# Kernel tuning notes

Hardware: AMD Instinct MI355X
Metric: run time of the kernel (lower is better)

## Reference

```python
import jax, jax.numpy as jnp
import numpy as np

SR = 48000.0
STAB_EPS = 1e-3
BS = 32
N_FRAMES = 128
N_SAMPLES = 65536


def setup_inputs() -> dict:
    key = jax.random.key(0)
    ks = jax.random.split(key, 8)
    f0_hz = jax.random.uniform(ks[0], (BS,), minval=50.0, maxval=500.0)
    note_on_duration = jax.random.uniform(ks[1], (BS,), minval=0.3, maxval=1.0)
    phase = jax.random.uniform(ks[2], (BS,), minval=-np.pi, maxval=np.pi)
    logits = jax.random.normal(ks[3], (BS, N_FRAMES, 5))
    osc_shape = jax.random.uniform(ks[4], (BS,))
    osc_gain = jax.random.uniform(ks[5], (BS,), minval=0.5, maxval=1.0)
    dist_gain = jax.random.uniform(ks[6], (BS,), minval=1.0, maxval=4.0)
    learned_alpha = jax.random.uniform(ks[7], (BS,), minval=0.5, maxval=3.0)
    return dict(f0_hz=f0_hz, note_on_duration=note_on_duration, phase=phase,
                logits=logits, osc_shape=osc_shape, osc_gain=osc_gain,
                dist_gain=dist_gain, learned_alpha=learned_alpha,
                n_samples=N_SAMPLES)


def lin_interp_dim1(x, n_out):
    """Linear interpolation along dim 1 with align_corners=True. x: (bs, n_in, c)."""
    n_in = x.shape[1]
    pos = jnp.linspace(0.0, n_in - 1.0, n_out)
    i0 = jnp.floor(pos).astype(jnp.int32)
    i1 = jnp.minimum(i0 + 1, n_in - 1)
    frac = (pos - i0.astype(x.dtype))[None, :, None]
    return x[:, i0] * (1.0 - frac) + x[:, i1] * frac


def square_saw_vco(f0_hz, osc_shape, n_samples, phase):
    """torchsynth-style square/saw morph oscillator. f0_hz, osc_shape, phase: (bs,)."""
    f0 = f0_hz[:, None]                                   # (bs, 1)
    inc = jnp.broadcast_to(f0 / SR, (f0.shape[0], n_samples))
    arg = 2.0 * jnp.pi * jnp.cumsum(inc, axis=1) + phase[:, None]
    partials = 12000.0 / (f0 * jnp.log10(f0))
    square = jnp.tanh(jnp.pi * partials * jnp.sin(arg) / 2.0)
    s = osc_shape[:, None]
    return (1.0 - s / 2.0) * square * (1.0 + s * jnp.cos(arg / 2.0))


def exp_decay_env(alpha, note_on_duration, n_samples):
    t = jnp.arange(n_samples, dtype=jnp.float32) / SR     # (n,)
    ramp = jnp.clip(1.0 - t[None, :] / note_on_duration[:, None], STAB_EPS, 1.0)
    env = ramp ** alpha[:, None]
    return jnp.where(t[None, :] <= note_on_duration[:, None], env, 0.0)


def logits_to_a_coeff_triangle(a_logits):
    """Map 2 logits to a stable biquad denominator (a1, a2) inside the stability triangle."""
    stab = 1.0 - STAB_EPS
    a1 = 2.0 * jnp.tanh(a_logits[..., 0]) * stab
    a1_abs = jnp.abs(a1)
    a2 = ((2.0 - a1_abs) * jnp.tanh(a_logits[..., 1]) * stab + a1_abs) / 2.0
    return jnp.stack([a1, a2], axis=-1)


def sample_wise_lpc(x, a):
    """Time-varying all-pole order-2: y[t] = x[t] - a1[t]*y[t-1] - a2[t]*y[t-2].
    x: (bs, n), a: (bs, n, 2). Sequential lax.scan over time."""
    def step(carry, inp):
        y1, y2 = carry
        xt, a1, a2 = inp
        y = xt - a1 * y1 - a2 * y2
        return (y, y1), y
    z = jnp.zeros(x.shape[0], dtype=x.dtype)
    xs = (x.T, a[..., 0].T, a[..., 1].T)                  # time-major
    _, ys = jax.lax.scan(step, (z, z), xs)
    return ys.T


def time_varying_fir(x, b):
    """y[t] = b0[t]*x[t] + b1[t]*x[t-1] + b2[t]*x[t-2], zero initial state."""
    x1 = jnp.pad(x, ((0, 0), (1, 0)))[:, :-1]
    x2 = jnp.pad(x, ((0, 0), (2, 0)))[:, :-2]
    return b[..., 0] * x + b[..., 1] * x1 + b[..., 2] * x2


def reference(f0_hz, note_on_duration, phase, logits, osc_shape, osc_gain,
              dist_gain, learned_alpha, n_samples):
    # --- oscillator + envelope ---
    dry = square_saw_vco(f0_hz, osc_shape, n_samples, phase)
    dry = dry * osc_gain[:, None]
    envelope = exp_decay_env(learned_alpha, note_on_duration, n_samples)
    dry = dry * envelope
    # --- coefficients (interp_logits=False: map to coeffs at frame rate, then upsample) ---
    a_coeff = logits_to_a_coeff_triangle(logits[..., :2])   # (bs, n_frames, 2)
    b_coeff = logits[..., 2:]                                # (bs, n_frames, 3)
    a_coeff = lin_interp_dim1(a_coeff, n_samples)            # (bs, n, 2)
    b_coeff = lin_interp_dim1(b_coeff, n_samples)            # (bs, n, 3)
    # --- time-varying biquad: all-pole recursion then FIR ---
    y_a = sample_wise_lpc(dry, a_coeff)
    y_ab = time_varying_fir(y_a, b_coeff)
    # --- distortion ---
    wet = jnp.tanh(y_ab * dist_gain[:, None])
    a0 = jnp.ones_like(a_coeff[:, :, 0])
    a_coeff3 = jnp.stack([a0, a_coeff[:, :, 0], a_coeff[:, :, 1]], axis=2)
    return (dry, wet, envelope, y_ab, a_coeff3, b_coeff, y_a)
```

## Files before the change

### kernel.cpp

```cpp
#include <hip/hip_runtime.h>
#include <cmath>

#define DI __device__ __forceinline__

constexpr int BS = 32;
constexpr int NS = 65536;
constexpr int NF = 128;
constexpr int CH = 256;
constexpr int NC = NS / CH;
constexpr size_t U = (size_t)BS * NS;
constexpr double PI_D = 3.14159265358979323846;
constexpr float STAB = 0.999f;

struct M6 { float a, b, c, d, u, v; };

DI M6 comp(const M6& R, const M6& L) {
    M6 o;
    o.a = fmaf(R.a, L.a, R.b * L.c);
    o.b = fmaf(R.a, L.b, R.b * L.d);
    o.c = fmaf(R.c, L.a, R.d * L.c);
    o.d = fmaf(R.c, L.b, R.d * L.d);
    o.u = fmaf(R.a, L.u, fmaf(R.b, L.v, R.u));
    o.v = fmaf(R.c, L.u, fmaf(R.d, L.v, R.v));
    return o;
}

DI void wave_scan6(M6& s, int lane) {
    #pragma unroll
    for (int d = 1; d < 64; d <<= 1) {
        M6 o;
        o.a = __shfl_up(s.a, d, 64); o.b = __shfl_up(s.b, d, 64);
        o.c = __shfl_up(s.c, d, 64); o.d = __shfl_up(s.d, d, 64);
        o.u = __shfl_up(s.u, d, 64); o.v = __shfl_up(s.v, d, 64);
        M6 t = comp(s, o);
        bool p = lane >= d;
        s.a = p ? t.a : s.a; s.b = p ? t.b : s.b; s.c = p ? t.c : s.c;
        s.d = p ? t.d : s.d; s.u = p ? t.u : s.u; s.v = p ? t.v : s.v;
    }
}

DI M6 ld6(const float* p) { M6 m; m.a=p[0]; m.b=p[1]; m.c=p[2]; m.d=p[3]; m.u=p[4]; m.v=p[5]; return m; }
DI void st6(float* p, const M6& m) { p[0]=m.a; p[1]=m.b; p[2]=m.c; p[3]=m.d; p[4]=m.u; p[5]=m.v; }

DI M6 block_scan6(M6 s, float (*wt)[6], int tid) {
    int lane = tid & 63, w = tid >> 6;
    wave_scan6(s, lane);
    if (lane == 63) st6(wt[w], s);
    __syncthreads();
    if (w > 0) {
        M6 p = ld6(wt[0]);
        for (int i = 1; i < w; i++) p = comp(ld6(wt[i]), p);
        s = comp(s, p);
    }
    return s;
}

DI void ipos(int t, int& i0, int& i1, float& fr) {
    double pos = (double)t * (127.0 / 65535.0);
    int p0 = (int)pos;
    i0 = p0;
    i1 = (p0 + 1 > 127) ? 127 : p0 + 1;
    fr = (float)(pos - (double)p0);
}

DI float fast_tanh(float x) {
    float e = __expf(2.0f * x);
    return 1.0f - 2.0f / (e + 1.0f);
}

DI void stage_frames(const float* __restrict__ logits, int b, int F, int tid,
                     float (*sfa)[2], float (*sfb)[3]) {
    if (tid < 3) {
        int fidx = F + tid; if (fidx > 127) fidx = 127;
        const float* L = logits + (size_t)(b * NF + fidx) * 5;
        float a1 = 2.0f * tanhf(L[0]) * STAB;
        float aa = fabsf(a1);
        float a2 = ((2.0f - aa) * tanhf(L[1]) * STAB + aa) * 0.5f;
        sfa[tid][0] = a1; sfa[tid][1] = a2;
        sfb[tid][0] = L[2]; sfb[tid][1] = L[3]; sfb[tid][2] = L[4];
    }
}

__global__ __launch_bounds__(CH) void k_osc(
    const float* __restrict__ f0_hz, const float* __restrict__ note_dur,
    const float* __restrict__ phase, const float* __restrict__ logits,
    const float* __restrict__ osc_shape, const float* __restrict__ osc_gain,
    const float* __restrict__ alpha,
    float* __restrict__ ws_chunk, float* __restrict__ out) {
    __shared__ float sfa[3][2], sfb[3][3], wt[4][6];
    const int bid = blockIdx.x;
    const int b = bid / NC, c = bid % NC;
    const int tid = threadIdx.x;
    const int t = c * CH + tid;
    const size_t g = (size_t)b * NS + t;
    const int F = (int)((double)(c * CH) * (127.0 / 65535.0));

    stage_frames(logits, b, F, tid, sfa, sfb);

    const float f0 = f0_hz[b];
    const float ph = phase[b];
    const float sh = osc_shape[b];
    const float gn = osc_gain[b];
    const float dur = note_dur[b];
    const float al = alpha[b];

    const double inc = (double)f0 / 48000.0;
    const double cum = (double)(t + 1) * inc;
    const double uu = cum - 2.0 * floor(cum * 0.5);
    const float theta = (float)(PI_D * uu + 0.5 * (double)ph);
    float sn, cs;
    __sincosf(theta, &sn, &cs);
    const float partials = 12000.0f / (f0 * __log10f(f0));
    const float sq = fast_tanh(1.57079632679f * partials * (2.0f * sn * cs));
    const float dry0 = (1.0f - 0.5f * sh) * sq * (1.0f + sh * cs);

    const float tsec = (float)t * (1.0f / 48000.0f);
    float env = 0.0f;
    if (tsec <= dur) {
        float ramp = 1.0f - tsec / dur;
        ramp = ramp < 0.001f ? 0.001f : (ramp > 1.0f ? 1.0f : ramp);
        env = __expf(al * __logf(ramp));
    }
    const float dry = dry0 * gn * env;

    __syncthreads();

    int i0, i1; float fr;
    ipos(t, i0, i1, fr);
    const float w0 = 1.0f - fr;
    const int l0 = i0 - F, l1 = i1 - F;
    const float a1i = sfa[l0][0] * w0 + sfa[l1][0] * fr;
    const float a2i = sfa[l0][1] * w0 + sfa[l1][1] * fr;
    const float b0 = sfb[l0][0] * w0 + sfb[l1][0] * fr;
    const float b1 = sfb[l0][1] * w0 + sfb[l1][1] * fr;
    const float b2 = sfb[l0][2] * w0 + sfb[l1][2] * fr;

    out[g] = dry;
    out[2 * U + g] = env;
    float* a3 = out + 4 * U;
    a3[g * 3 + 0] = 1.0f; a3[g * 3 + 1] = a1i; a3[g * 3 + 2] = a2i;
    float* bco = out + 7 * U;
    bco[g * 3 + 0] = b0; bco[g * 3 + 1] = b1; bco[g * 3 + 2] = b2;

    M6 m; m.a = -a1i; m.b = -a2i; m.c = 1.0f; m.d = 0.0f; m.u = dry; m.v = 0.0f;
    const int lane = tid & 63, w = tid >> 6;
    wave_scan6(m, lane);
    if (lane == 63) st6(wt[w], m);
    __syncthreads();
    if (tid == 255) {
        M6 p = ld6(wt[0]);
        p = comp(ld6(wt[1]), p);
        p = comp(ld6(wt[2]), p);
        M6 tot = comp(m, p);
        st6(ws_chunk + ((size_t)b * NC + c) * 6, tot);
    }
}

__global__ __launch_bounds__(CH) void k_iir(
    const float* __restrict__ logits, const float* __restrict__ dist_gain,
    const float* __restrict__ ws_chunk, float* __restrict__ out) {
    __shared__ float sfa[3][2], sfb[3][3], wtA[4][6], wtB[4][6];
    __shared__ float sv[CH][2], sy[CH];
    const int bid = blockIdx.x;
    const int b = bid / NC, c = bid % NC;
    const int tid = threadIdx.x;
    const int t = c * CH + tid;
    const size_t g = (size_t)b * NS + t;
    const int F = (int)((double)(c * CH) * (127.0 / 65535.0));

    stage_frames(logits, b, F, tid, sfa, sfb);

    M6 csum = ld6(ws_chunk + ((size_t)b * NC + tid) * 6);
    M6 inc = block_scan6(csum, wtA, tid);
    sv[tid][0] = inc.u; sv[tid][1] = inc.v;
    __syncthreads();
    const float s0 = (c == 0) ? 0.0f : sv[c - 1][0];
    const float s1 = (c == 0) ? 0.0f : sv[c - 1][1];

    int i0, i1; float fr;
    ipos(t, i0, i1, fr);
    const float w0 = 1.0f - fr;
    const int l0 = i0 - F, l1 = i1 - F;
    const float a1i = sfa[l0][0] * w0 + sfa[l1][0] * fr;
    const float a2i = sfa[l0][1] * w0 + sfa[l1][1] * fr;
    const float b0 = sfb[l0][0] * w0 + sfb[l1][0] * fr;
    const float b1 = sfb[l0][1] * w0 + sfb[l1][1] * fr;
    const float b2 = sfb[l0][2] * w0 + sfb[l1][2] * fr;
    const float x = out[g];

    M6 m; m.a = -a1i; m.b = -a2i; m.c = 1.0f; m.d = 0.0f; m.u = x; m.v = 0.0f;
    M6 f = block_scan6(m, wtB, tid);
    const float y = fmaf(f.a, s0, fmaf(f.b, s1, f.u));
    sy[tid] = y;
    __syncthreads();

    const float ym1 = (tid >= 1) ? sy[tid - 1] : s0;
    const float ym2 = (tid >= 2) ? sy[tid - 2] : ((tid == 1) ? s0 : s1);
    const float yab = b0 * y + b1 * ym1 + b2 * ym2;
    const float wet = fast_tanh(yab * dist_gain[b]);
    out[U + g] = wet;
    out[3 * U + g] = yab;
    out[10 * U + g] = y;
}

extern "C" void kernel_launch(void* const* d_in, const int* in_sizes, int n_in,
                              void* d_out, int out_size, void* d_ws, size_t ws_size,
                              hipStream_t stream) {
    const float* f0   = (const float*)d_in[0];
    const float* dur  = (const float*)d_in[1];
    const float* ph   = (const float*)d_in[2];
    const float* lg   = (const float*)d_in[3];
    const float* shp  = (const float*)d_in[4];
    const float* gn   = (const float*)d_in[5];
    const float* dist = (const float*)d_in[6];
    const float* alp  = (const float*)d_in[7];
    float* out = (float*)d_out;
    float* ws_chunk = (float*)d_ws;

    k_osc<<<BS * NC, CH, 0, stream>>>(f0, dur, ph, lg, shp, gn, alp, ws_chunk, out);
    k_iir<<<BS * NC, CH, 0, stream>>>(lg, dist, ws_chunk, out);
}
```

Baseline: 155.3 us.

## Process four samples per thread with serial local recurrence and vectorized stores

Each thread now handles four consecutive samples. Within a thread the biquad recursion runs serially to build a local affine transform, and the wave and block scan then combines these per-thread transforms, which cuts shuffle-scan work and block count by a factor of four. The chunk-prefix scan in the IIR kernel becomes a single 64-lane wave scan, since there are only 64 chunks per batch item. Outputs are written with float4 stores, including the packed 3-channel coefficient arrays. More registers are used per thread, and an exclusive-prefix shuffle is needed to recover each thread's starting state.

```diff
diff --git a/kernel.cpp b/kernel.cpp
--- a/kernel.cpp
+++ b/kernel.cpp
@@ -6,8 +6,10 @@
 constexpr int BS = 32;
 constexpr int NS = 65536;
 constexpr int NF = 128;
-constexpr int CH = 256;
-constexpr int NC = NS / CH;
+constexpr int S  = 4;
+constexpr int TB = 256;
+constexpr int SAMP = TB * S;
+constexpr int NC = NS / SAMP;
 constexpr size_t U = (size_t)BS * NS;
 constexpr double PI_D = 3.14159265358979323846;
 constexpr float STAB = 0.999f;
@@ -25,6 +27,14 @@
     return o;
 }
 
+DI void stepL(M6& A, float a1, float a2, float x) {
+    float na = fmaf(-a1, A.a, -a2 * A.c);
+    float nb = fmaf(-a1, A.b, -a2 * A.d);
+    float nu = fmaf(-a1, A.u, fmaf(-a2, A.v, x));
+    A.c = A.a; A.d = A.b; A.v = A.u;
+    A.a = na;  A.b = nb;  A.u = nu;
+}
+
 DI void wave_scan6(M6& s, int lane) {
     #pragma unroll
     for (int d = 1; d < 64; d <<= 1) {
@@ -42,19 +52,6 @@
 DI M6 ld6(const float* p) { M6 m; m.a=p[0]; m.b=p[1]; m.c=p[2]; m.d=p[3]; m.u=p[4]; m.v=p[5]; return m; }
 DI void st6(float* p, const M6& m) { p[0]=m.a; p[1]=m.b; p[2]=m.c; p[3]=m.d; p[4]=m.u; p[5]=m.v; }
 
-DI M6 block_scan6(M6 s, float (*wt)[6], int tid) {
-    int lane = tid & 63, w = tid >> 6;
-    wave_scan6(s, lane);
-    if (lane == 63) st6(wt[w], s);
-    __syncthreads();
-    if (w > 0) {
-        M6 p = ld6(wt[0]);
-        for (int i = 1; i < w; i++) p = comp(ld6(wt[i]), p);
-        s = comp(s, p);
-    }
-    return s;
-}
-
 DI void ipos(int t, int& i0, int& i1, float& fr) {
     double pos = (double)t * (127.0 / 65535.0);
     int p0 = (int)pos;
@@ -70,7 +67,7 @@
 
 DI void stage_frames(const float* __restrict__ logits, int b, int F, int tid,
                      float (*sfa)[2], float (*sfb)[3]) {
-    if (tid < 3) {
+    if (tid < 4) {
         int fidx = F + tid; if (fidx > 127) fidx = 127;
         const float* L = logits + (size_t)(b * NF + fidx) * 5;
         float a1 = 2.0f * tanhf(L[0]) * STAB;
@@ -81,19 +78,35 @@
     }
 }
 
-__global__ __launch_bounds__(CH) void k_osc(
+DI void interp4(int t0, int F, const float (*sfa)[2], const float (*sfb)[3],
+                float* a1v, float* a2v, float* b0v, float* b1v, float* b2v) {
+    #pragma unroll
+    for (int k = 0; k < S; k++) {
+        int i0, i1; float fr;
+        ipos(t0 + k, i0, i1, fr);
+        float w0 = 1.0f - fr;
+        int l0 = i0 - F, l1 = i1 - F;
+        a1v[k] = sfa[l0][0] * w0 + sfa[l1][0] * fr;
+        a2v[k] = sfa[l0][1] * w0 + sfa[l1][1] * fr;
+        b0v[k] = sfb[l0][0] * w0 + sfb[l1][0] * fr;
+        b1v[k] = sfb[l0][1] * w0 + sfb[l1][1] * fr;
+        b2v[k] = sfb[l0][2] * w0 + sfb[l1][2] * fr;
+    }
+}
+
+__global__ __launch_bounds__(TB) void k_osc(
     const float* __restrict__ f0_hz, const float* __restrict__ note_dur,
     const float* __restrict__ phase, const float* __restrict__ logits,
     const float* __restrict__ osc_shape, const float* __restrict__ osc_gain,
     const float* __restrict__ alpha,
     float* __restrict__ ws_chunk, float* __restrict__ out) {
-    __shared__ float sfa[3][2], sfb[3][3], wt[4][6];
+    __shared__ float sfa[4][2], sfb[4][3], wt[4][6];
     const int bid = blockIdx.x;
     const int b = bid / NC, c = bid % NC;
     const int tid = threadIdx.x;
-    const int t = c * CH + tid;
-    const size_t g = (size_t)b * NS + t;
-    const int F = (int)((double)(c * CH) * (127.0 / 65535.0));
+    const int t0 = c * SAMP + tid * S;
+    const size_t g0 = (size_t)b * NS + t0;
+    const int F = (int)((double)(c * SAMP) * (127.0 / 65535.0));
 
     stage_frames(logits, b, F, tid, sfa, sfb);
 
@@ -103,104 +116,133 @@
     const float gn = osc_gain[b];
     const float dur = note_dur[b];
     const float al = alpha[b];
-
     const double inc = (double)f0 / 48000.0;
-    const double cum = (double)(t + 1) * inc;
-    const double uu = cum - 2.0 * floor(cum * 0.5);
-    const float theta = (float)(PI_D * uu + 0.5 * (double)ph);
-    float sn, cs;
-    __sincosf(theta, &sn, &cs);
     const float partials = 12000.0f / (f0 * __log10f(f0));
-    const float sq = fast_tanh(1.57079632679f * partials * (2.0f * sn * cs));
-    const float dry0 = (1.0f - 0.5f * sh) * sq * (1.0f + sh * cs);
-
-    const float tsec = (float)t * (1.0f / 48000.0f);
-    float env = 0.0f;
-    if (tsec <= dur) {
-        float ramp = 1.0f - tsec / dur;
-        ramp = ramp < 0.001f ? 0.001f : (ramp > 1.0f ? 1.0f : ramp);
-        env = __expf(al * __logf(ramp));
-    }
-    const float dry = dry0 * gn * env;
-
-    __syncthreads();
-
-    int i0, i1; float fr;
-    ipos(t, i0, i1, fr);
-    const float w0 = 1.0f - fr;
-    const int l0 = i0 - F, l1 = i1 - F;
-    const float a1i = sfa[l0][0] * w0 + sfa[l1][0] * fr;
-    const float a2i = sfa[l0][1] * w0 + sfa[l1][1] * fr;
-    const float b0 = sfb[l0][0] * w0 + sfb[l1][0] * fr;
-    const float b1 = sfb[l0][1] * w0 + sfb[l1][1] * fr;
-    const float b2 = sfb[l0][2] * w0 + sfb[l1][2] * fr;
-
-    out[g] = dry;
-    out[2 * U + g] = env;
-    float* a3 = out + 4 * U;
-    a3[g * 3 + 0] = 1.0f; a3[g * 3 + 1] = a1i; a3[g * 3 + 2] = a2i;
-    float* bco = out + 7 * U;
-    bco[g * 3 + 0] = b0; bco[g * 3 + 1] = b1; bco[g * 3 + 2] = b2;
-
-    M6 m; m.a = -a1i; m.b = -a2i; m.c = 1.0f; m.d = 0.0f; m.u = dry; m.v = 0.0f;
+
+    float x[S], env4[S];
+    #pragma unroll
+    for (int k = 0; k < S; k++) {
+        int t = t0 + k;
+        double cum = (double)(t + 1) * inc;
+        double uu = cum - 2.0 * floor(cum * 0.5);
+        float theta = (float)(PI_D * uu + 0.5 * (double)ph);
+        float sn, cs;
+        __sincosf(theta, &sn, &cs);
+        float sq = fast_tanh(1.57079632679f * partials * (2.0f * sn * cs));
+        float dry0 = (1.0f - 0.5f * sh) * sq * (1.0f + sh * cs);
+        float tsec = (float)t * (1.0f / 48000.0f);
+        float env = 0.0f;
+        if (tsec <= dur) {
+            float ramp = 1.0f - tsec / dur;
+            ramp = ramp < 0.001f ? 0.001f : (ramp > 1.0f ? 1.0f : ramp);
+            env = __expf(al * __logf(ramp));
+        }
+        env4[k] = env;
+        x[k] = dry0 * gn * env;
+    }
+    __syncthreads();
+
+    float a1v[S], a2v[S], b0v[S], b1v[S], b2v[S];
+    interp4(t0, F, sfa, sfb, a1v, a2v, b0v, b1v, b2v);
+
+    *(float4*)&out[g0]         = make_float4(x[0], x[1], x[2], x[3]);
+    *(float4*)&out[2 * U + g0] = make_float4(env4[0], env4[1], env4[2], env4[3]);
+    float* a3 = out + 4 * U + g0 * 3;
+    *(float4*)&a3[0] = make_float4(1.0f, a1v[0], a2v[0], 1.0f);
+    *(float4*)&a3[4] = make_float4(a1v[1], a2v[1], 1.0f, a1v[2]);
+    *(float4*)&a3[8] = make_float4(a2v[2], 1.0f, a1v[3], a2v[3]);
+    float* bc = out + 7 * U + g0 * 3;
+    *(float4*)&bc[0] = make_float4(b0v[0], b1v[0], b2v[0], b0v[1]);
+    *(float4*)&bc[4] = make_float4(b1v[1], b2v[1], b0v[2], b1v[2]);
+    *(float4*)&bc[8] = make_float4(b2v[2], b0v[3], b1v[3], b2v[3]);
+
+    M6 A; A.a = -a1v[0]; A.b = -a2v[0]; A.c = 1.0f; A.d = 0.0f; A.u = x[0]; A.v = 0.0f;
+    #pragma unroll
+    for (int k = 1; k < S; k++) stepL(A, a1v[k], a2v[k], x[k]);
+
     const int lane = tid & 63, w = tid >> 6;
-    wave_scan6(m, lane);
-    if (lane == 63) st6(wt[w], m);
-    __syncthreads();
-    if (tid == 255) {
+    wave_scan6(A, lane);
+    if (lane == 63) st6(wt[w], A);
+    __syncthreads();
+    if (tid == TB - 1) {
         M6 p = ld6(wt[0]);
         p = comp(ld6(wt[1]), p);
         p = comp(ld6(wt[2]), p);
-        M6 tot = comp(m, p);
+        M6 tot = comp(A, p);
         st6(ws_chunk + ((size_t)b * NC + c) * 6, tot);
     }
 }
 
-__global__ __launch_bounds__(CH) void k_iir(
+__global__ __launch_bounds__(TB) void k_iir(
     const float* __restrict__ logits, const float* __restrict__ dist_gain,
     const float* __restrict__ ws_chunk, float* __restrict__ out) {
-    __shared__ float sfa[3][2], sfb[3][3], wtA[4][6], wtB[4][6];
-    __shared__ float sv[CH][2], sy[CH];
+    __shared__ float sfa[4][2], sfb[4][3], wt[4][6], sv[NC][2];
     const int bid = blockIdx.x;
     const int b = bid / NC, c = bid % NC;
     const int tid = threadIdx.x;
-    const int t = c * CH + tid;
-    const size_t g = (size_t)b * NS + t;
-    const int F = (int)((double)(c * CH) * (127.0 / 65535.0));
+    const int t0 = c * SAMP + tid * S;
+    const size_t g0 = (size_t)b * NS + t0;
+    const int F = (int)((double)(c * SAMP) * (127.0 / 65535.0));
 
     stage_frames(logits, b, F, tid, sfa, sfb);
 
-    M6 csum = ld6(ws_chunk + ((size_t)b * NC + tid) * 6);
-    M6 inc = block_scan6(csum, wtA, tid);
-    sv[tid][0] = inc.u; sv[tid][1] = inc.v;
-    __syncthreads();
-    const float s0 = (c == 0) ? 0.0f : sv[c - 1][0];
-    const float s1 = (c == 0) ? 0.0f : sv[c - 1][1];
-
-    int i0, i1; float fr;
-    ipos(t, i0, i1, fr);
-    const float w0 = 1.0f - fr;
-    const int l0 = i0 - F, l1 = i1 - F;
-    const float a1i = sfa[l0][0] * w0 + sfa[l1][0] * fr;
-    const float a2i = sfa[l0][1] * w0 + sfa[l1][1] * fr;
-    const float b0 = sfb[l0][0] * w0 + sfb[l1][0] * fr;
-    const float b1 = sfb[l0][1] * w0 + sfb[l1][1] * fr;
-    const float b2 = sfb[l0][2] * w0 + sfb[l1][2] * fr;
-    const float x = out[g];
-
-    M6 m; m.a = -a1i; m.b = -a2i; m.c = 1.0f; m.d = 0.0f; m.u = x; m.v = 0.0f;
-    M6 f = block_scan6(m, wtB, tid);
-    const float y = fmaf(f.a, s0, fmaf(f.b, s1, f.u));
-    sy[tid] = y;
-    __syncthreads();
-
-    const float ym1 = (tid >= 1) ? sy[tid - 1] : s0;
-    const float ym2 = (tid >= 2) ? sy[tid - 2] : ((tid == 1) ? s0 : s1);
-    const float yab = b0 * y + b1 * ym1 + b2 * ym2;
-    const float wet = fast_tanh(yab * dist_gain[b]);
-    out[U + g] = wet;
-    out[3 * U + g] = yab;
-    out[10 * U + g] = y;
+    if (tid < NC) {
+        M6 cs = ld6(ws_chunk + ((size_t)b * NC + tid) * 6);
+        wave_scan6(cs, tid);
+        sv[tid][0] = cs.u; sv[tid][1] = cs.v;
+    }
+
+    float4 xv = *(const float4*)&out[g0];
+    float x[S] = {xv.x, xv.y, xv.z, xv.w};
+
+    __syncthreads();
+    const float s0 = c ? sv[c - 1][0] : 0.0f;
+    const float s1 = c ? sv[c - 1][1] : 0.0f;
+
+    float a1v[S], a2v[S], b0v[S], b1v[S], b2v[S];
+    interp4(t0, F, sfa, sfb, a1v, a2v, b0v, b1v, b2v);
+
+    M6 A; A.a = -a1v[0]; A.b = -a2v[0]; A.c = 1.0f; A.d = 0.0f; A.u = x[0]; A.v = 0.0f;
+    #pragma unroll
+    for (int k = 1; k < S; k++) stepL(A, a1v[k], a2v[k], x[k]);
+
+    const int lane = tid & 63, w = tid >> 6;
+    wave_scan6(A, lane);
+    if (lane == 63) st6(wt[w], A);
+    __syncthreads();
+
+    M6 P; P.a = 1.f; P.b = 0.f; P.c = 0.f; P.d = 1.f; P.u = 0.f; P.v = 0.f;
+    for (int i = 0; i < w; i++) P = comp(ld6(wt[i]), P);
+    M6 prev;
+    prev.a = __shfl_up(A.a, 1, 64); prev.b = __shfl_up(A.b, 1, 64);
+    prev.c = __shfl_up(A.c, 1, 64); prev.d = __shfl_up(A.d, 1, 64);
+    prev.u = __shfl_up(A.u, 1, 64); prev.v = __shfl_up(A.v, 1, 64);
+    M6 E = (lane == 0) ? P : comp(prev, P);
+
+    float y1 = fmaf(E.a, s0, fmaf(E.b, s1, E.u));
+    float y2 = fmaf(E.c, s0, fmaf(E.d, s1, E.v));
+    const float ys0 = y1, ys1 = y2;
+
+    float y[S];
+    #pragma unroll
+    for (int k = 0; k < S; k++) {
+        y[k] = fmaf(-a1v[k], y1, fmaf(-a2v[k], y2, x[k]));
+        y2 = y1; y1 = y[k];
+    }
+
+    const float dg = dist_gain[b];
+    float yab[S], wet[S];
+    #pragma unroll
+    for (int k = 0; k < S; k++) {
+        float ym1 = (k >= 1) ? y[k - 1] : ys0;
+        float ym2 = (k >= 2) ? y[k - 2] : ((k == 1) ? ys0 : ys1);
+        yab[k] = b0v[k] * y[k] + b1v[k] * ym1 + b2v[k] * ym2;
+        wet[k] = fast_tanh(yab[k] * dg);
+    }
+
+    *(float4*)&out[U + g0]      = make_float4(wet[0], wet[1], wet[2], wet[3]);
+    *(float4*)&out[3 * U + g0]  = make_float4(yab[0], yab[1], yab[2], yab[3]);
+    *(float4*)&out[10 * U + g0] = make_float4(y[0], y[1], y[2], y[3]);
 }
 
 extern "C" void kernel_launch(void* const* d_in, const int* in_sizes, int n_in,
@@ -217,6 +259,6 @@
     float* out = (float*)d_out;
     float* ws_chunk = (float*)d_ws;
 
-    k_osc<<<BS * NC, CH, 0, stream>>>(f0, dur, ph, lg, shp, gn, alp, ws_chunk, out);
-    k_iir<<<BS * NC, CH, 0, stream>>>(lg, dist, ws_chunk, out);
-}
+    k_osc<<<BS * NC, TB, 0, stream>>>(f0, dur, ph, lg, shp, gn, alp, ws_chunk, out);
+    k_iir<<<BS * NC, TB, 0, stream>>>(lg, dist, ws_chunk, out);
+}
```

New measurement: 131.9 us. -15.1%, faster.
